# Optimization experiments

Hardware: AMD Instinct MI355X
Metric: run time of the kernel (lower is better)

The kernel has to match this reference:

```python
import jax, jax.numpy as jnp
import numpy as np

B, T, C = 4, 2048, 1024
H = 16
D = C // H  # head_size = 64


def setup_inputs() -> dict:
    key = jax.random.key(0)
    ks = jax.random.split(key, 5)
    s = 0.02
    return {
        "x": jax.random.normal(ks[0], (B, T, C), dtype=jnp.float32),
        "Wq": jax.random.normal(ks[1], (C, C), dtype=jnp.float32) * s,
        "Wk": jax.random.normal(ks[2], (C, C), dtype=jnp.float32) * s,
        "Wv": jax.random.normal(ks[3], (C, C), dtype=jnp.float32) * s,
        "Wp": jax.random.normal(ks[4], (C, C), dtype=jnp.float32) * s,
        "bp": jnp.zeros((C,), dtype=jnp.float32),
    }


def reference(x, Wq, Wk, Wv, Wp, bp):
    Bq, Tq, Cq = x.shape
    # torch Linear: y = x @ W.T ; split into heads [B, H, T, D]
    def split(y):
        return y.reshape(Bq, Tq, H, D).transpose(0, 2, 1, 3)
    q = split(x @ Wq.T)
    k = split(x @ Wk.T)
    v = split(x @ Wv.T)
    # NOTE: original scales by C**-0.5 (full n_embed), not head_size**-0.5
    scale = Cq ** (-0.5)
    att = jnp.einsum('bhqd,bhkd->bhqk', q, k) * scale  # [B,H,T,T]
    causal = jnp.tril(jnp.ones((Tq, Tq), dtype=bool))
    att = jnp.where(causal[None, None, :, :], att, -jnp.inf)
    att = jax.nn.softmax(att, axis=-1)
    out = jnp.einsum('bhqk,bhkd->bhqd', att, v)  # [B,H,T,D]
    out = out.transpose(0, 2, 1, 3).reshape(Bq, Tq, Cq)
    return out @ Wp.T + bp
```

## Files before the change

### kernel.cpp

```cpp
#include <hip/hip_runtime.h>
#include <cstdint>
#include <cstddef>

typedef __attribute__((ext_vector_type(8))) __bf16 bf16x8;
typedef __attribute__((ext_vector_type(4))) __bf16 bf16x4;
typedef __attribute__((ext_vector_type(4))) float f32x4;
typedef __attribute__((ext_vector_type(16))) float f32x16;
typedef __attribute__((ext_vector_type(4))) unsigned uint4v;

#define B_ 4
#define T_ 2048
#define C_ 1024
#define H_ 16
#define D_ 64
#define NTILES_ (T_ / 32)
#define TILE_ELEMS_ 2048
#define BH_STRIDE_ ((size_t)NTILES_ * TILE_ELEMS_)

__device__ __forceinline__ float fexp2(float x) {
#if __has_builtin(__builtin_amdgcn_exp2f)
  return __builtin_amdgcn_exp2f(x);
#else
  return __expf(x * 0.69314718f);
#endif
}

__global__ __launch_bounds__(256) void castall(
    const float* __restrict__ x, const float* __restrict__ wq, const float* __restrict__ wk,
    const float* __restrict__ wv, const float* __restrict__ wp,
    __bf16* __restrict__ xb, __bf16* __restrict__ wqb, __bf16* __restrict__ wkb,
    __bf16* __restrict__ wvb, __bf16* __restrict__ wpb) {
  const int bid = blockIdx.x;
  const float* src;
  __bf16* dst;
  if (bid < 8192)       { src = x  + (size_t)bid * 1024;           dst = xb  + (size_t)bid * 1024; }
  else if (bid < 9216)  { src = wq + (size_t)(bid - 8192) * 1024;  dst = wqb + (size_t)(bid - 8192) * 1024; }
  else if (bid < 10240) { src = wk + (size_t)(bid - 9216) * 1024;  dst = wkb + (size_t)(bid - 9216) * 1024; }
  else if (bid < 11264) { src = wv + (size_t)(bid - 10240) * 1024; dst = wvb + (size_t)(bid - 10240) * 1024; }
  else                  { src = wp + (size_t)(bid - 11264) * 1024; dst = wpb + (size_t)(bid - 11264) * 1024; }
  const int i = threadIdx.x * 4;
  float4 f = *reinterpret_cast<const float4*>(src + i);
  bf16x4 o;
  o[0] = (__bf16)f.x; o[1] = (__bf16)f.y; o[2] = (__bf16)f.z; o[3] = (__bf16)f.w;
  *reinterpret_cast<bf16x4*>(dst + i) = o;
}

__device__ __forceinline__ void gload_lds16(const __bf16* g, __bf16* lds) {
  __builtin_amdgcn_global_load_lds(
      (const __attribute__((address_space(1))) void*)g,
      (__attribute__((address_space(3))) void*)lds, 16, 0, 0);
}

#define ST_A41(BUFO, KT, HH)                                                          \
  do {                                                                                \
    const __bf16* s0_ = Agp + (size_t)(m0 + (HH) * 128 + srow) * 1024 + (KT) * 64 + sswz; \
    gload_lds16(s0_, LDSb + (BUFO) + (HH) * 8192 + w * 1024);                         \
    gload_lds16(s0_ + 8 * 1024, LDSb + (BUFO) + (HH) * 8192 + w * 1024 + 512);        \
  } while (0)
#define ST_B41(BUFO, KT)                                                              \
  do {                                                                                \
    const __bf16* s0_ = Bgp + (size_t)(n0 + srow) * 1024 + (KT) * 64 + sswz;          \
    gload_lds16(s0_, LDSb + 32768 + (BUFO) + w * 1024);                               \
    gload_lds16(s0_ + 8 * 1024, LDSb + 32768 + (BUFO) + w * 1024 + 512);              \
  } while (0)
#define RDA41(M, KK) (*reinterpret_cast<const bf16x8*>(                               \
    LDSb + bufoA + (wr * 64 + (M) * 16 + lr) * 64 + (((KK) * 32 + lg * 8) ^ ((lr & 7) * 8))))
#define RDB41(N, KK) (*reinterpret_cast<const bf16x8*>(                               \
    LDSb + 32768 + bufoB + (wc * 64 + (N) * 16 + lr) * 64 + (((KK) * 32 + lg * 8) ^ ((lr & 7) * 8))))

#define GEMM8_KLOOP_41                                                                \
  ST_A41(0, 0, 0); ST_A41(0, 0, 1); ST_B41(0, 0);                                     \
  __builtin_amdgcn_sched_barrier(0);                                                  \
  asm volatile("s_waitcnt vmcnt(0)" ::: "memory");                                    \
  __builtin_amdgcn_s_barrier();                                                       \
  __builtin_amdgcn_sched_barrier(0);                                                  \
  for (int t = 0; t < 16; ++t) {                                                      \
    const int bufoA = (t & 1) * 16384;                                                \
    const int bufoB = (t & 1) * 8192;                                                 \
    const int nboA = ((t + 1) & 1) * 16384;                                           \
    const int nboB = ((t + 1) & 1) * 8192;                                            \
    const bool st = t < 15;                                                           \
    afA[0][0] = RDA41(0, 0); afA[0][1] = RDA41(0, 1);                                 \
    afA[1][0] = RDA41(1, 0); afA[1][1] = RDA41(1, 1);                                 \
    bfA[0][0] = RDB41(0, 0); bfA[0][1] = RDB41(0, 1);                                 \
    bfA[1][0] = RDB41(1, 0); bfA[1][1] = RDB41(1, 1);                                 \
    if (st) ST_A41(nboA, t + 1, 0);                                                   \
    __builtin_amdgcn_s_setprio(1);                                                    \
    _Pragma("unroll")                                                                 \
    for (int kk = 0; kk < 2; ++kk)                                                    \
      _Pragma("unroll")                                                               \
      for (int m = 0; m < 2; ++m) {                                                   \
        acc[m][0] = __builtin_amdgcn_mfma_f32_16x16x32_bf16(afA[m][kk], bfA[0][kk], acc[m][0], 0, 0, 0); \
        acc[m][1] = __builtin_amdgcn_mfma_f32_16x16x32_bf16(afA[m][kk], bfA[1][kk], acc[m][1], 0, 0, 0); \
      }                                                                               \
    __builtin_amdgcn_s_setprio(0);                                                    \
    __builtin_amdgcn_s_barrier();                                                     \
    bfB[0][0] = RDB41(2, 0); bfB[0][1] = RDB41(2, 1);                                 \
    bfB[1][0] = RDB41(3, 0); bfB[1][1] = RDB41(3, 1);                                 \
    if (st) ST_A41(nboA, t + 1, 1);                                                   \
    __builtin_amdgcn_s_setprio(1);                                                    \
    _Pragma("unroll")                                                                 \
    for (int kk = 0; kk < 2; ++kk)                                                    \
      _Pragma("unroll")                                                               \
      for (int m = 0; m < 2; ++m) {                                                   \
        acc[m][2] = __builtin_amdgcn_mfma_f32_16x16x32_bf16(afA[m][kk], bfB[0][kk], acc[m][2], 0, 0, 0); \
        acc[m][3] = __builtin_amdgcn_mfma_f32_16x16x32_bf16(afA[m][kk], bfB[1][kk], acc[m][3], 0, 0, 0); \
      }                                                                               \
    __builtin_amdgcn_s_setprio(0);                                                    \
    __builtin_amdgcn_s_barrier();                                                     \
    afB[0][0] = RDA41(2, 0); afB[0][1] = RDA41(2, 1);                                 \
    afB[1][0] = RDA41(3, 0); afB[1][1] = RDA41(3, 1);                                 \
    if (st) ST_B41(nboB, t + 1);                                                      \
    __builtin_amdgcn_s_setprio(1);                                                    \
    _Pragma("unroll")                                                                 \
    for (int kk = 0; kk < 2; ++kk)                                                    \
      _Pragma("unroll")                                                               \
      for (int m = 0; m < 2; ++m) {                                                   \
        acc[m + 2][0] = __builtin_amdgcn_mfma_f32_16x16x32_bf16(afB[m][kk], bfA[0][kk], acc[m + 2][0], 0, 0, 0); \
        acc[m + 2][1] = __builtin_amdgcn_mfma_f32_16x16x32_bf16(afB[m][kk], bfA[1][kk], acc[m + 2][1], 0, 0, 0); \
      }                                                                               \
    __builtin_amdgcn_s_setprio(0);                                                    \
    __builtin_amdgcn_s_barrier();                                                     \
    __builtin_amdgcn_s_setprio(1);                                                    \
    _Pragma("unroll")                                                                 \
    for (int kk = 0; kk < 2; ++kk)                                                    \
      _Pragma("unroll")                                                               \
      for (int m = 0; m < 2; ++m) {                                                   \
        acc[m + 2][2] = __builtin_amdgcn_mfma_f32_16x16x32_bf16(afB[m][kk], bfB[0][kk], acc[m + 2][2], 0, 0, 0); \
        acc[m + 2][3] = __builtin_amdgcn_mfma_f32_16x16x32_bf16(afB[m][kk], bfB[1][kk], acc[m + 2][3], 0, 0, 0); \
      }                                                                               \
    __builtin_amdgcn_s_setprio(0);                                                    \
    __builtin_amdgcn_sched_barrier(0);                                                \
    asm volatile("s_waitcnt vmcnt(0)" ::: "memory");                                  \
    __builtin_amdgcn_s_barrier();                                                     \
    __builtin_amdgcn_sched_barrier(0);                                                \
  }

__global__ __launch_bounds__(512, 2) void gemm_qkv8(
    const __bf16* __restrict__ Agp, const __bf16* __restrict__ Bgp,
    __bf16* __restrict__ qf, __bf16* __restrict__ kf, __bf16* __restrict__ vf) {
  __shared__ __bf16 LDSb[49152];
  const int tid = threadIdx.x;
  const int w = tid >> 6, l = tid & 63;
  const int wr = w >> 1, wc = w & 1;
  const int lr = l & 15, lg = l >> 4;
  int lin = blockIdx.y * 24 + blockIdx.x;
  lin = (lin & 7) * 96 + (lin >> 3);
  const int bx = lin % 24, by = lin / 24;
  const int m0 = by * 256, n0 = bx * 128;
  const int srow = w * 16 + (l >> 3);
  const int sswz = ((l & 7) ^ ((l >> 3) & 7)) * 8;

  f32x4 acc[4][4] = {};
  bf16x8 afA[2][2], afB[2][2], bfA[2][2], bfB[2][2];

  GEMM8_KLOOP_41

  __bf16* wl = LDSb + w * 4096;
  const int colb = n0 + wc * 64;
  const int mat = colb >> 10;
  const int h = (colb >> 6) & 15;
  const int b = m0 >> 11;
  const float qsc = (mat == 0) ? 0.04508422f : 1.0f;
#pragma unroll
  for (int mi = 0; mi < 4; ++mi) {
    const int rt = mi >> 1;
#pragma unroll
    for (int n = 0; n < 4; ++n) {
      const int d = n * 16 + lr;
#pragma unroll
      for (int j = 0; j < 4; ++j) {
        const int rowloc = (mi & 1) * 16 + lg * 4 + j;
        int off;
        if (mat < 2)
          off = ((d >> 4) & 3) * 512 + ((d >> 3) & 1) * 256 + rowloc * 8 + (d & 7);
        else
          off = (d >> 5) * 1024 + ((rowloc >> 4) & 1) * 512 + ((rowloc >> 3) & 1) * 256 +
                (d & 31) * 8 + (rowloc & 7);
        wl[rt * 2048 + off] = (__bf16)(acc[mi][n][j] * qsc);
      }
    }
  }
  __bf16* dstbase = (mat == 0 ? qf : mat == 1 ? kf : vf) + (size_t)(b * 16 + h) * BH_STRIDE_;
  const int rt0 = ((m0 + wr * 64) >> 5) & 63;
#pragma unroll
  for (int rt = 0; rt < 2; ++rt)
#pragma unroll
    for (int c = 0; c < 4; ++c) {
      const bf16x8 vchunk = *reinterpret_cast<const bf16x8*>(wl + rt * 2048 + c * 512 + l * 8);
      *reinterpret_cast<bf16x8*>(dstbase + (size_t)(rt0 + rt) * TILE_ELEMS_ + c * 512 + l * 8) = vchunk;
    }
}

__global__ __launch_bounds__(512, 2) void gemm_proj8(
    const __bf16* __restrict__ Agp, const __bf16* __restrict__ Bgp,
    float* __restrict__ out, const float* __restrict__ bias) {
  __shared__ __bf16 LDSb[49152];
  const int tid = threadIdx.x;
  const int w = tid >> 6, l = tid & 63;
  const int wr = w >> 1, wc = w & 1;
  const int lr = l & 15, lg = l >> 4;
  int lin = blockIdx.y * 8 + blockIdx.x;
  lin = (lin & 7) * 32 + (lin >> 3);
  const int bx = lin & 7, by = lin >> 3;
  const int m0 = by * 256, n0 = bx * 128;
  const int srow = w * 16 + (l >> 3);
  const int sswz = ((l & 7) ^ ((l >> 3) & 7)) * 8;

  f32x4 acc[4][4] = {};
  bf16x8 afA[2][2], afB[2][2], bfA[2][2], bfB[2][2];

  GEMM8_KLOOP_41

  const int colb = n0 + wc * 64;
#pragma unroll
  for (int mi = 0; mi < 4; ++mi) {
    const int row = m0 + wr * 64 + mi * 16 + lg * 4;
#pragma unroll
    for (int n = 0; n < 4; ++n) {
      const int col = colb + n * 16 + lr;
      const float bv = bias[col];
#pragma unroll
      for (int j = 0; j < 4; ++j)
        out[(size_t)(row + j) * 1024 + col] = acc[mi][n][j] + bv;
    }
  }
}

__device__ __forceinline__ unsigned pk2(float a, float b) {
  const unsigned short ua = __builtin_bit_cast(unsigned short, (__bf16)a);
  const unsigned short ub = __builtin_bit_cast(unsigned short, (__bf16)b);
  return (unsigned)ua | ((unsigned)ub << 16);
}

__device__ __forceinline__ void exch2(unsigned X, unsigned Y, int hi,
                                      unsigned& w0, unsigned& w2) {
#if __has_builtin(__builtin_amdgcn_permlane32_swap)
  auto r = __builtin_amdgcn_permlane32_swap(X, Y, false, false);
  w0 = r[0];
  w2 = r[1];
#else
  const unsigned sX = __shfl_xor(X, 32);
  const unsigned sY = __shfl_xor(Y, 32);
  w0 = hi ? sY : X;
  w2 = hi ? Y : sX;
#endif
}

#define LOADKV(SFX, TT)                                                          \
  do {                                                                           \
    const __bf16* kp_ = kfb + (size_t)(TT) * TILE_ELEMS_ + lx8;                  \
    k##SFX##0 = *reinterpret_cast<const bf16x8*>(kp_);                           \
    k##SFX##1 = *reinterpret_cast<const bf16x8*>(kp_ + 512);                     \
    k##SFX##2 = *reinterpret_cast<const bf16x8*>(kp_ + 1024);                    \
    k##SFX##3 = *reinterpret_cast<const bf16x8*>(kp_ + 1536);                    \
    const __bf16* vp_ = vfb + (size_t)(TT) * TILE_ELEMS_ + lx8;                  \
    v##SFX##0 = *reinterpret_cast<const bf16x8*>(vp_);                           \
    v##SFX##1 = *reinterpret_cast<const bf16x8*>(vp_ + 512);                     \
    v##SFX##2 = *reinterpret_cast<const bf16x8*>(vp_ + 1024);                    \
    v##SFX##3 = *reinterpret_cast<const bf16x8*>(vp_ + 1536);                    \
  } while (0)

#define TILE(SFX, MASKED)                                                        \
  do {                                                                           \
    f32x16 s = {};                                                               \
    s = __builtin_amdgcn_mfma_f32_32x32x16_bf16(k##SFX##0, qf[0], s, 0, 0, 0);   \
    s = __builtin_amdgcn_mfma_f32_32x32x16_bf16(k##SFX##1, qf[1], s, 0, 0, 0);   \
    s = __builtin_amdgcn_mfma_f32_32x32x16_bf16(k##SFX##2, qf[2], s, 0, 0, 0);   \
    s = __builtin_amdgcn_mfma_f32_32x32x16_bf16(k##SFX##3, qf[3], s, 0, 0, 0);   \
    float sv[16];                                                                \
    _Pragma("unroll") for (int r = 0; r < 16; ++r) sv[r] = s[r];                 \
    if (MASKED) {                                                                \
      _Pragma("unroll") for (int r = 0; r < 16; ++r) {                           \
        const int kvloc = (r & 3) + 8 * (r >> 2) + 4 * hi;                       \
        sv[r] = (kvloc <= lane31) ? sv[r] : -1e30f;                              \
      }                                                                          \
    }                                                                            \
    _Pragma("unroll") for (int r = 0; r < 16; ++r) sv[r] = fexp2(sv[r]);         \
    unsigned pwv[8];                                                             \
    _Pragma("unroll") for (int ks = 0; ks < 2; ++ks) {                           \
      const unsigned X0 = pk2(sv[ks * 8 + 0], sv[ks * 8 + 1]);                   \
      const unsigned X1 = pk2(sv[ks * 8 + 2], sv[ks * 8 + 3]);                   \
      const unsigned Y0 = pk2(sv[ks * 8 + 4], sv[ks * 8 + 5]);                   \
      const unsigned Y1 = pk2(sv[ks * 8 + 6], sv[ks * 8 + 7]);                   \
      exch2(X0, Y0, hi, pwv[ks * 4 + 0], pwv[ks * 4 + 2]);                       \
      exch2(X1, Y1, hi, pwv[ks * 4 + 1], pwv[ks * 4 + 3]);                       \
    }                                                                            \
    const uint4v u0 = {pwv[0], pwv[1], pwv[2], pwv[3]};                          \
    const uint4v u1 = {pwv[4], pwv[5], pwv[6], pwv[7]};                          \
    const bf16x8 pf0 = __builtin_bit_cast(bf16x8, u0);                           \
    const bf16x8 pf1 = __builtin_bit_cast(bf16x8, u1);                           \
    acc0 = __builtin_amdgcn_mfma_f32_32x32x16_bf16(v##SFX##0, pf0, acc0, 0, 0, 0); \
    acc0 = __builtin_amdgcn_mfma_f32_32x32x16_bf16(v##SFX##1, pf1, acc0, 0, 0, 0); \
    acc1 = __builtin_amdgcn_mfma_f32_32x32x16_bf16(v##SFX##2, pf0, acc1, 0, 0, 0); \
    acc1 = __builtin_amdgcn_mfma_f32_32x32x16_bf16(v##SFX##3, pf1, acc1, 0, 0, 0); \
    float b8[8];                                                                 \
    _Pragma("unroll") for (int r = 0; r < 8; ++r) b8[r] = sv[2 * r] + sv[2 * r + 1]; \
    _Pragma("unroll") for (int r = 0; r < 4; ++r) b8[r] = b8[2 * r] + b8[2 * r + 1]; \
    l_run += (b8[0] + b8[1]) + (b8[2] + b8[3]);                                  \
  } while (0)

__global__ __launch_bounds__(512) void attn_fwd(const __bf16* __restrict__ qfr,
                                                const __bf16* __restrict__ kfr,
                                                const __bf16* __restrict__ vfr,
                                                __bf16* __restrict__ ao) {
  __shared__ float Pls[4 * 64 * 34];
  const int tid = threadIdx.x;
  const int w = tid >> 6, l = tid & 63;
  const int p = w >> 1, hf = w & 1;
  const int lane31 = l & 31, hi = l >> 5;
  const int bh = blockIdx.x & 63;
  const int qi = blockIdx.x >> 6;
  const int b = bh >> 4;
  const int qx = qi * 4 + p;
  const size_t rowbase = (size_t)b * T_;
  const int hoff = (bh & 15) * D_;
  const int lx8 = l * 8;
  const __bf16* qfb = qfr + (size_t)bh * BH_STRIDE_;
  const __bf16* kfb = kfr + (size_t)bh * BH_STRIDE_;
  const __bf16* vfb = vfr + (size_t)bh * BH_STRIDE_;
  float* pb = Pls + p * (64 * 34) + l * 34;

  for (int phase = 0; phase < 2; ++phase) {
    const int qg = (phase ? 63 - qx : qx) * 32;
    const int ntiles = (qg >> 5) + 1;
    const int nh = ntiles >> 1;
    const int tb = hf ? nh : 0;
    const int te = hf ? ntiles : nh;
    const int nt = te - tb;
    const bool dm = (hf == 1);

    bf16x8 qf[4];
    {
      const __bf16* qp = qfb + (size_t)(qg >> 5) * TILE_ELEMS_ + lx8;
#pragma unroll
      for (int t4 = 0; t4 < 4; ++t4) qf[t4] = *reinterpret_cast<const bf16x8*>(qp + t4 * 512);
    }

    f32x16 acc0 = {};
    f32x16 acc1 = {};
    float l_run = 0.f;

    bf16x8 kA0, kA1, kA2, kA3, vA0, vA1, vA2, vA3;
    bf16x8 kB0, kB1, kB2, kB3, vB0, vB1, vB2, vB3;

    if (nt > 0) {
      LOADKV(A, tb);
      int i = 0;
      for (; i + 1 < nt; ++i) {
        if ((i & 1) == 0) { LOADKV(B, tb + i + 1); TILE(A, false); }
        else              { LOADKV(A, tb + i + 1); TILE(B, false); }
      }
      if ((i & 1) == 0) TILE(A, dm);
      else              TILE(B, dm);
    }

    if (hf) {
#pragma unroll
      for (int r = 0; r < 16; ++r) { pb[r] = acc0[r]; pb[16 + r] = acc1[r]; }
      pb[32] = l_run;
    }
    __syncthreads();
    if (!hf) {
#pragma unroll
      for (int r = 0; r < 16; ++r) { acc0[r] += pb[r]; acc1[r] += pb[16 + r]; }
      l_run += pb[32];
      l_run += __shfl_xor(l_run, 32);
      const float rl = 1.0f / l_run;
      __bf16* op = ao + (rowbase + qg + lane31) * C_ + hoff + hi * 4;
#pragma unroll
      for (int dblk = 0; dblk < 2; ++dblk)
#pragma unroll
        for (int qd = 0; qd < 4; ++qd) {
          bf16x4 ov;
#pragma unroll
          for (int j = 0; j < 4; ++j) {
            const float av = (dblk == 0) ? acc0[qd * 4 + j] : acc1[qd * 4 + j];
            ov[j] = (__bf16)(av * rl);
          }
          *reinterpret_cast<bf16x4*>(op + dblk * 32 + qd * 8) = ov;
        }
    }
    __syncthreads();
  }
}

extern "C" void kernel_launch(void* const* d_in, const int* in_sizes, int n_in,
                              void* d_out, int out_size, void* d_ws, size_t ws_size,
                              hipStream_t stream) {
  const float* x  = (const float*)d_in[0];
  const float* Wq = (const float*)d_in[1];
  const float* Wk = (const float*)d_in[2];
  const float* Wv = (const float*)d_in[3];
  const float* Wp = (const float*)d_in[4];
  const float* bp = (const float*)d_in[5];
  float* out = (float*)d_out;

  const int NX = B_ * T_ * C_;
  const int NW = C_ * C_;

  __bf16* xb  = (__bf16*)d_ws;
  __bf16* wqb = xb + NX;
  __bf16* wkb = wqb + NW;
  __bf16* wvb = wkb + NW;
  __bf16* wpb = wvb + NW;
  __bf16* qf  = wpb + NW;
  __bf16* kf  = qf + NX;
  __bf16* vf  = kf + NX;
  __bf16* aob = xb;

  castall<<<12288, 256, 0, stream>>>(x, Wq, Wk, Wv, Wp, xb, wqb, wkb, wvb, wpb);

  gemm_qkv8<<<dim3(24, 32), 512, 0, stream>>>(xb, wqb, qf, kf, vf);
  attn_fwd<<<512, 512, 0, stream>>>(qf, kf, vf, aob);
  gemm_proj8<<<dim3(8, 32), 512, 0, stream>>>(aob, wpb, out, bp);
}
```

Measured before the change: 157.4 us.

## Drop split-KV wave pairs in attention, one wave per query tile

Attention previously split each 32-row query tile's KV range across two waves and merged their partial accumulators through shared memory with block barriers. Now each wave handles a whole query tile's KV range alone, with blocks of 256 threads. This removes the LDS reduction and both __syncthreads, but halves total wave count and doubles per-wave serial KV work, which lowers latency hiding and parallelism.

```diff
diff --git a/kernel.cpp b/kernel.cpp
--- a/kernel.cpp
+++ b/kernel.cpp
@@ -300,35 +300,27 @@
     l_run += (b8[0] + b8[1]) + (b8[2] + b8[3]);                                  \
   } while (0)
 
-__global__ __launch_bounds__(512) void attn_fwd(const __bf16* __restrict__ qfr,
+__global__ __launch_bounds__(256) void attn_fwd(const __bf16* __restrict__ qfr,
                                                 const __bf16* __restrict__ kfr,
                                                 const __bf16* __restrict__ vfr,
                                                 __bf16* __restrict__ ao) {
-  __shared__ float Pls[4 * 64 * 34];
   const int tid = threadIdx.x;
   const int w = tid >> 6, l = tid & 63;
-  const int p = w >> 1, hf = w & 1;
   const int lane31 = l & 31, hi = l >> 5;
   const int bh = blockIdx.x & 63;
   const int qi = blockIdx.x >> 6;
   const int b = bh >> 4;
-  const int qx = qi * 4 + p;
+  const int qx = qi * 4 + w;
   const size_t rowbase = (size_t)b * T_;
   const int hoff = (bh & 15) * D_;
   const int lx8 = l * 8;
   const __bf16* qfb = qfr + (size_t)bh * BH_STRIDE_;
   const __bf16* kfb = kfr + (size_t)bh * BH_STRIDE_;
   const __bf16* vfb = vfr + (size_t)bh * BH_STRIDE_;
-  float* pb = Pls + p * (64 * 34) + l * 34;
 
   for (int phase = 0; phase < 2; ++phase) {
     const int qg = (phase ? 63 - qx : qx) * 32;
     const int ntiles = (qg >> 5) + 1;
-    const int nh = ntiles >> 1;
-    const int tb = hf ? nh : 0;
-    const int te = hf ? ntiles : nh;
-    const int nt = te - tb;
-    const bool dm = (hf == 1);
 
     bf16x8 qf[4];
     {
@@ -344,44 +336,31 @@
     bf16x8 kA0, kA1, kA2, kA3, vA0, vA1, vA2, vA3;
     bf16x8 kB0, kB1, kB2, kB3, vB0, vB1, vB2, vB3;
 
-    if (nt > 0) {
-      LOADKV(A, tb);
-      int i = 0;
-      for (; i + 1 < nt; ++i) {
-        if ((i & 1) == 0) { LOADKV(B, tb + i + 1); TILE(A, false); }
-        else              { LOADKV(A, tb + i + 1); TILE(B, false); }
+    LOADKV(A, 0);
+    int t = 0;
+    for (; t + 1 < ntiles; ++t) {
+      if ((t & 1) == 0) { LOADKV(B, t + 1); TILE(A, false); }
+      else              { LOADKV(A, t + 1); TILE(B, false); }
+    }
+    if ((t & 1) == 0) TILE(A, true);
+    else              TILE(B, true);
+
+    l_run += __shfl_xor(l_run, 32);
+
+    const float rl = 1.0f / l_run;
+    __bf16* op = ao + (rowbase + qg + lane31) * C_ + hoff + hi * 4;
+#pragma unroll
+    for (int dblk = 0; dblk < 2; ++dblk)
+#pragma unroll
+      for (int qd = 0; qd < 4; ++qd) {
+        bf16x4 ov;
+#pragma unroll
+        for (int j = 0; j < 4; ++j) {
+          const float av = (dblk == 0) ? acc0[qd * 4 + j] : acc1[qd * 4 + j];
+          ov[j] = (__bf16)(av * rl);
+        }
+        *reinterpret_cast<bf16x4*>(op + dblk * 32 + qd * 8) = ov;
       }
-      if ((i & 1) == 0) TILE(A, dm);
-      else              TILE(B, dm);
-    }
-
-    if (hf) {
-#pragma unroll
-      for (int r = 0; r < 16; ++r) { pb[r] = acc0[r]; pb[16 + r] = acc1[r]; }
-      pb[32] = l_run;
-    }
-    __syncthreads();
-    if (!hf) {
-#pragma unroll
-      for (int r = 0; r < 16; ++r) { acc0[r] += pb[r]; acc1[r] += pb[16 + r]; }
-      l_run += pb[32];
-      l_run += __shfl_xor(l_run, 32);
-      const float rl = 1.0f / l_run;
-      __bf16* op = ao + (rowbase + qg + lane31) * C_ + hoff + hi * 4;
-#pragma unroll
-      for (int dblk = 0; dblk < 2; ++dblk)
-#pragma unroll
-        for (int qd = 0; qd < 4; ++qd) {
-          bf16x4 ov;
-#pragma unroll
-          for (int j = 0; j < 4; ++j) {
-            const float av = (dblk == 0) ? acc0[qd * 4 + j] : acc1[qd * 4 + j];
-            ov[j] = (__bf16)(av * rl);
-          }
-          *reinterpret_cast<bf16x4*>(op + dblk * 32 + qd * 8) = ov;
-        }
-    }
-    __syncthreads();
   }
 }
 
@@ -412,6 +391,6 @@
   castall<<<12288, 256, 0, stream>>>(x, Wq, Wk, Wv, Wp, xb, wqb, wkb, wvb, wpb);
 
   gemm_qkv8<<<dim3(24, 32), 512, 0, stream>>>(xb, wqb, qf, kf, vf);
-  attn_fwd<<<512, 512, 0, stream>>>(qf, kf, vf, aob);
+  attn_fwd<<<512, 256, 0, stream>>>(qf, kf, vf, aob);
   gemm_proj8<<<dim3(8, 32), 512, 0, stream>>>(aob, wpb, out, bp);
 }
```

After: 157.5 us, median of 2. No clear change (+0.0%).
